# Performance work log

Hardware: AMD Instinct MI355X
Metric: run time of the kernel (lower is better)

## Reference

```python
import jax, jax.numpy as jnp
import numpy as np

SHAPES = ((64, 64), (32, 32), (16, 16), (8, 8))
LEVEL_STARTS = np.concatenate([[0], np.cumsum([h * w for h, w in SHAPES])]).tolist()
N_LEVELS = 4; N_HEADS = 8; N_POINTS = 4; D_MODEL = 256; HEAD_DIM = 32; D_FFN = 1024; NUM_LAYERS = 2
LEN_IN = sum(h * w for h, w in SHAPES)
BATCH = 2


def setup_inputs():
    key = jax.random.key(0)
    ks = iter(jax.random.split(key, 40))
    r = lambda shape, s=1.0: jax.random.normal(next(ks), shape, dtype=jnp.float32) * s
    L = NUM_LAYERS
    return {
        "src": r((BATCH, LEN_IN, D_MODEL)),
        "pos": r((BATCH, LEN_IN, D_MODEL), 0.5),
        "valid_ratios": jnp.ones((BATCH, N_LEVELS, 2), jnp.float32),
        "Wv": r((L, D_MODEL, D_MODEL), 0.05), "bv": jnp.zeros((L, D_MODEL), jnp.float32),
        "Woff": r((L, D_MODEL, N_HEADS * N_LEVELS * N_POINTS * 2), 0.002),
        "boff": r((L, N_HEADS * N_LEVELS * N_POINTS * 2), 0.5),
        "Wa": r((L, D_MODEL, N_HEADS * N_LEVELS * N_POINTS), 0.05),
        "ba": jnp.zeros((L, N_HEADS * N_LEVELS * N_POINTS), jnp.float32),
        "Wo": r((L, D_MODEL, D_MODEL), 0.05), "bo": jnp.zeros((L, D_MODEL), jnp.float32),
        "g1": jnp.ones((L, D_MODEL), jnp.float32), "be1": jnp.zeros((L, D_MODEL), jnp.float32),
        "Wl1": r((L, D_MODEL, D_FFN), 0.05), "bl1": jnp.zeros((L, D_FFN), jnp.float32),
        "Wl2": r((L, D_FFN, D_MODEL), 0.05), "bl2": jnp.zeros((L, D_MODEL), jnp.float32),
        "g2": jnp.ones((L, D_MODEL), jnp.float32), "be2": jnp.zeros((L, D_MODEL), jnp.float32),
    }


def layer_norm(x, g, b, eps=1e-5):
    m = jnp.mean(x, -1, keepdims=True)
    v = jnp.mean(jnp.square(x - m), -1, keepdims=True)
    return (x - m) * jax.lax.rsqrt(v + eps) * g + b


def make_reference_points(valid_ratios):
    # DeformableTransformerEncoder.get_reference_points, vectorized per level
    refs = []
    for lvl, (H, W) in enumerate(SHAPES):
        gy, gx = jnp.meshgrid(jnp.arange(H, dtype=jnp.float32) + 0.5,
                              jnp.arange(W, dtype=jnp.float32) + 0.5, indexing="ij")
        ry = gy.reshape(-1)[None] / (valid_ratios[:, lvl, 1][:, None] * H)
        rx = gx.reshape(-1)[None] / (valid_ratios[:, lvl, 0][:, None] * W)
        refs.append(jnp.stack([rx, ry], -1))  # [N, H*W, 2]
    ref = jnp.concatenate(refs, 1)  # [N, Len, 2]
    return ref[:, :, None, :] * valid_ratios[:, None]  # [N, Len, n_levels, 2]


def ms_deform_attn(query, input_flatten, reference_points, Wv, bv, Woff, boff, Wa, ba, Wo, bo):
    N, Lq, _ = query.shape
    value = (input_flatten @ Wv + bv).reshape(N, -1, N_HEADS, HEAD_DIM)
    off = (query @ Woff + boff).reshape(N, Lq, N_HEADS, N_LEVELS, N_POINTS, 2)
    aw = (query @ Wa + ba).reshape(N, Lq, N_HEADS, N_LEVELS * N_POINTS)
    aw = jax.nn.softmax(aw, -1).reshape(N, Lq, N_HEADS, N_LEVELS, N_POINTS)
    # normalizer is (W, H) per level, as in MSDeformAttn
    normalizer = jnp.array([[w, h] for h, w in SHAPES], jnp.float32)
    loc = reference_points[:, :, None, :, None, :] + off / normalizer[None, None, None, :, None, :]
    acc = jnp.zeros((N, N_HEADS, Lq, HEAD_DIM), query.dtype)
    for lvl, (H, W) in enumerate(SHAPES):
        s = LEVEL_STARTS[lvl]
        val = value[:, s:s + H * W].transpose(0, 2, 1, 3)  # [N, heads, H*W, hd]
        # grid_sample bilinear, align_corners=False, zero padding
        x = loc[:, :, :, lvl, :, 0] * W - 0.5  # [N, Lq, heads, P]
        y = loc[:, :, :, lvl, :, 1] * H - 0.5
        x0 = jnp.floor(x); y0 = jnp.floor(y)
        wx1 = x - x0; wy1 = y - y0
        ix0 = x0.astype(jnp.int32); iy0 = y0.astype(jnp.int32)

        def corner(ix, iy, w):
            valid = (ix >= 0) & (ix < W) & (iy >= 0) & (iy < H)
            idx = jnp.clip(iy, 0, H - 1) * W + jnp.clip(ix, 0, W - 1)
            idx = idx.transpose(0, 2, 1, 3).reshape(N, N_HEADS, Lq * N_POINTS)
            g = jnp.take_along_axis(val, idx[..., None], axis=2).reshape(N, N_HEADS, Lq, N_POINTS, HEAD_DIM)
            w = jnp.where(valid, w, 0.0).transpose(0, 2, 1, 3)  # [N, heads, Lq, P]
            return g * w[..., None]

        sampled = (corner(ix0, iy0, (1 - wx1) * (1 - wy1))
                   + corner(ix0 + 1, iy0, wx1 * (1 - wy1))
                   + corner(ix0, iy0 + 1, (1 - wx1) * wy1)
                   + corner(ix0 + 1, iy0 + 1, wx1 * wy1))
        acc = acc + (sampled * aw[:, :, :, lvl].transpose(0, 2, 1, 3)[..., None]).sum(3)
    out = acc.transpose(0, 2, 1, 3).reshape(N, Lq, D_MODEL)
    return out @ Wo + bo


def reference(src, pos, valid_ratios, Wv, bv, Woff, boff, Wa, ba, Wo, bo,
              g1, be1, Wl1, bl1, Wl2, bl2, g2, be2):
    ref_pts = make_reference_points(valid_ratios)
    out = src
    for l in range(NUM_LAYERS):
        q = out + pos  # with_pos_embed
        attn = ms_deform_attn(q, out, ref_pts, Wv[l], bv[l], Woff[l], boff[l],
                              Wa[l], ba[l], Wo[l], bo[l])
        out = layer_norm(out + attn, g1[l], be1[l])
        ffn = jax.nn.relu(out @ Wl1[l] + bl1[l]) @ Wl2[l] + bl2[l]
        out = layer_norm(out + ffn, g2[l], be2[l])
    return out
```

## Files before the change

### kernel.cpp

```cpp
#include <hip/hip_runtime.h>
#include <math.h>

#define LEN   5440
#define NB    2
#define MROWS (NB * LEN)
#define DM    256
#define NH    8
#define HD    32
#define NLV   4
#define NPT   4
#define DFFN  1024

typedef __attribute__((ext_vector_type(8))) short bf16x8;
typedef __attribute__((ext_vector_type(4))) short bf16x4;
typedef __attribute__((ext_vector_type(4))) float f32x4;

__device__ __forceinline__ short f2bf(float f) {
    union { float f; unsigned u; } cv; cv.f = f;
    unsigned r = cv.u + 0x7fffu + ((cv.u >> 16) & 1u);
    return (short)(r >> 16);
}
__device__ __forceinline__ float bf2f(short s) {
    union { unsigned u; float f; } cv;
    cv.u = ((unsigned)(unsigned short)s) << 16;
    return cv.f;
}

__global__ __launch_bounds__(256) void transpose_convert_all(
    const float* __restrict__ Wv,  const float* __restrict__ Woff,
    const float* __restrict__ Wa,  const float* __restrict__ Wo,
    const float* __restrict__ Wl1, const float* __restrict__ Wl2,
    short* __restrict__ out)
{
    int bx = blockIdx.x;
    int l  = bx / 736;
    int t  = bx % 736;
    const float* src; int K, N; long doff;
    if      (t < 64)  { src = Wv;   K = 256;  N = 256;  doff = 0;      }
    else if (t < 128) { src = Woff; K = 256;  N = 256;  doff = 65536;  t -= 64;  }
    else if (t < 160) { src = Wa;   K = 256;  N = 128;  doff = 131072; t -= 128; }
    else if (t < 224) { src = Wo;   K = 256;  N = 256;  doff = 163840; t -= 160; }
    else if (t < 480) { src = Wl1;  K = 256;  N = 1024; doff = 229376; t -= 224; }
    else              { src = Wl2;  K = 1024; N = 256;  doff = 491520; t -= 480; }
    src += (long)l * K * N;
    short* dst = out + (long)l * 753664 + doff;

    const int ntx = N / 32;
    const int n0 = (t % ntx) * 32, k0 = (t / ntx) * 32;

    __shared__ short T[32][33];
    const int tid = threadIdx.x;
    {
        const int n = tid & 31, kq = tid >> 5;
        #pragma unroll
        for (int i = 0; i < 4; ++i) {
            int k = kq * 4 + i;
            T[n][k] = f2bf(src[(long)(k0 + k) * N + n0 + n]);
        }
    }
    __syncthreads();
    {
        const int k = tid & 31, nq = tid >> 5;
        #pragma unroll
        for (int i = 0; i < 4; ++i) {
            int n = nq * 4 + i;
            dst[(long)(n0 + n) * K + k0 + k] = T[n][k];
        }
    }
}

__global__ __launch_bounds__(256) void convert_src(
    const float4* __restrict__ s4, const float4* __restrict__ p4,
    bf16x4* __restrict__ curb, bf16x4* __restrict__ qb)
{
    const int i = blockIdx.x * 256 + threadIdx.x;
    float4 s = s4[i], p = p4[i];
    bf16x4 c, q;
    c[0] = f2bf(s.x); c[1] = f2bf(s.y); c[2] = f2bf(s.z); c[3] = f2bf(s.w);
    q[0] = f2bf(s.x + p.x); q[1] = f2bf(s.y + p.y);
    q[2] = f2bf(s.z + p.z); q[3] = f2bf(s.w + p.w);
    curb[i] = c; qb[i] = q;
}

template <int BN, int RELU, int OMODE>
__device__ __forceinline__ void gemm_core128(
    short* As, short* Bs,
    const short* __restrict__ A, const short* __restrict__ Wt,
    const float* __restrict__ bias, float* __restrict__ Cf,
    short* __restrict__ Cb,
    int ldc, int m0, int wrow0, int ccol0, int K)
{
    constexpr int NF = BN / 32;
    constexpr int NBJ = BN / 64;
    const int t    = threadIdx.x;
    const int wave = t >> 6, lane = t & 63;
    const int wm   = (wave & 1) * 64;
    const int wn   = (wave >> 1) * (BN / 2);
    const int lm   = lane & 15;
    const int chkg = lane >> 4;
    const int srow = t >> 2;
    const int sc   = t & 3;

    f32x4 acc[4][NF] = {};
    bf16x8 ar[2], br[NBJ];

    #pragma unroll
    for (int j = 0; j < 2; ++j)
        ar[j] = *(const bf16x8*)(A + (long)(m0 + srow + 64 * j) * K + sc * 8);
    #pragma unroll
    for (int j = 0; j < NBJ; ++j)
        br[j] = *(const bf16x8*)(Wt + (long)(wrow0 + srow + 64 * j) * K + sc * 8);

    for (int k0 = 0; k0 < K; k0 += 32) {
        __syncthreads();
        #pragma unroll
        for (int j = 0; j < 2; ++j)
            *(bf16x8*)(&As[(srow + 64 * j) * 40 + sc * 8]) = ar[j];
        #pragma unroll
        for (int j = 0; j < NBJ; ++j)
            *(bf16x8*)(&Bs[(srow + 64 * j) * 40 + sc * 8]) = br[j];
        __syncthreads();

        if (k0 + 32 < K) {
            #pragma unroll
            for (int j = 0; j < 2; ++j)
                ar[j] = *(const bf16x8*)(A + (long)(m0 + srow + 64 * j) * K + k0 + 32 + sc * 8);
            #pragma unroll
            for (int j = 0; j < NBJ; ++j)
                br[j] = *(const bf16x8*)(Wt + (long)(wrow0 + srow + 64 * j) * K + k0 + 32 + sc * 8);
        }

        bf16x8 af[4], bfv[NF];
        #pragma unroll
        for (int s = 0; s < 4; ++s)
            af[s] = *(const bf16x8*)(&As[(wm + s * 16 + lm) * 40 + chkg * 8]);
        #pragma unroll
        for (int u = 0; u < NF; ++u)
            bfv[u] = *(const bf16x8*)(&Bs[(wn + u * 16 + lm) * 40 + chkg * 8]);
        #pragma unroll
        for (int s = 0; s < 4; ++s)
            #pragma unroll
            for (int u = 0; u < NF; ++u)
                acc[s][u] = __builtin_amdgcn_mfma_f32_16x16x32_bf16(
                    af[s], bfv[u], acc[s][u], 0, 0, 0);
    }

    const int col = lane & 15;
    const int rq  = (lane >> 4) * 4;
    #pragma unroll
    for (int s = 0; s < 4; ++s) {
        #pragma unroll
        for (int u = 0; u < NF; ++u) {
            const int gn = ccol0 + wn + u * 16 + col;
            const float bb = bias[gn];
            #pragma unroll
            for (int r = 0; r < 4; ++r) {
                const int gm = m0 + wm + s * 16 + rq + r;
                float v = acc[s][u][r] + bb;
                if (RELU) v = fmaxf(v, 0.f);
                if (OMODE == 0) {
                    Cf[(long)gm * ldc + gn] = v;
                } else if (OMODE == 1) {
                    Cb[(long)gm * ldc + gn] = f2bf(v);
                } else {
                    const int n   = gm / LEN;
                    const int pix = gm - n * LEN;
                    const int h   = gn >> 5, d = gn & 31;
                    Cb[((long)(n * NH + h) * LEN + pix) * 32 + d] = f2bf(v);
                }
            }
        }
    }
}

template <int BN, int RELU, int OMODE>
__global__ __launch_bounds__(256) void gemm128(
    const short* __restrict__ A, const short* __restrict__ Wt,
    const float* __restrict__ bias, float* Cf, short* Cb, int ldc, int K)
{
    __shared__ __align__(16) short As[128 * 40];
    __shared__ __align__(16) short Bs[BN * 40];
    gemm_core128<BN, RELU, OMODE>(As, Bs, A, Wt, bias, Cf, Cb, ldc,
                                  blockIdx.y * 128, blockIdx.x * BN,
                                  blockIdx.x * BN, K);
}

__global__ __launch_bounds__(256) void gemm_qkv128(
    const short* __restrict__ curb, const short* __restrict__ qb,
    const short* __restrict__ Wt, const float* __restrict__ bv,
    const float* __restrict__ boff, const float* __restrict__ ba,
    short* __restrict__ Vb, float* __restrict__ OFF, float* __restrict__ AW)
{
    __shared__ __align__(16) short As[128 * 40];
    __shared__ __align__(16) short Bs[128 * 40];
    const int n0 = blockIdx.x * 128;
    if (n0 < 256) {
        gemm_core128<128, 0, 2>(As, Bs, curb, Wt, bv, (float*)nullptr, Vb,
                                256, blockIdx.y * 128, n0, n0, 256);
    } else if (n0 < 512) {
        gemm_core128<128, 0, 0>(As, Bs, qb, Wt, boff, OFF, (short*)nullptr,
                                256, blockIdx.y * 128, n0, n0 - 256, 256);
    } else {
        gemm_core128<128, 0, 0>(As, Bs, qb, Wt, ba, AW, (short*)nullptr,
                                128, blockIdx.y * 128, n0, n0 - 512, 256);
    }
}

__global__ __launch_bounds__(256) void deform_attn_v3(
    const short* __restrict__ Vb,
    const float* __restrict__ OFF,
    const float* __restrict__ AW,
    const float* __restrict__ vr,
    bf16x4* __restrict__ ATTb)
{
    const int starts[5] = {0, 4096, 5120, 5376, 5440};
    const int dims[4]   = {64, 32, 16, 8};

    const int wave = threadIdx.x >> 6;
    const int lane = threadIdx.x & 63;
    const int h    = lane >> 3;
    const int d4   = lane & 7;

    const int gq = blockIdx.x * 4 + wave;
    const int n  = gq / LEN;
    const int q  = gq % LEN;

    int lq = 3;
    if (q < 4096) lq = 0; else if (q < 5120) lq = 1; else if (q < 5376) lq = 2;
    const int r  = q - starts[lq];
    const int Wq = dims[lq];
    const int gy = r / Wq, gx = r % Wq;
    const float vrxq = vr[(n * NLV + lq) * 2 + 0];
    const float vryq = vr[(n * NLV + lq) * 2 + 1];
    const float rx = (gx + 0.5f) / (vrxq * Wq);
    const float ry = (gy + 0.5f) / (vryq * Wq);

    const long row = (long)n * LEN + q;

    const float* awp = AW + row * 128 + h * 16;
    float a[16];
    float mx = -1e30f;
    #pragma unroll
    for (int i = 0; i < 16; ++i) { a[i] = awp[i]; mx = fmaxf(mx, a[i]); }
    float s = 0.f;
    #pragma unroll
    for (int i = 0; i < 16; ++i) { a[i] = __expf(a[i] - mx); s += a[i]; }
    const float inv = 1.f / s;

    const float* offp = OFF + row * 256 + h * 32;

    float4 acc = {0.f, 0.f, 0.f, 0.f};
    #pragma unroll
    for (int lvl = 0; lvl < NLV; ++lvl) {
        const int Hl = dims[lvl];
        const int Wl = Hl;
        const float fW = (float)Wl;
        const int sb = starts[lvl];
        const float lx = rx * vr[(n * NLV + lvl) * 2 + 0];
        const float ly = ry * vr[(n * NLV + lvl) * 2 + 1];
        const short* vb = Vb + ((long)(n * NH + h) * LEN + sb) * 32 + d4 * 4;
        #pragma unroll
        for (int p = 0; p < NPT; ++p) {
            const float ox = offp[lvl * 8 + p * 2 + 0];
            const float oy = offp[lvl * 8 + p * 2 + 1];
            const float x = fmaf(lx, fW, ox) - 0.5f;
            const float y = fmaf(ly, fW, oy) - 0.5f;
            const float x0f = floorf(x), y0f = floorf(y);
            const int ix0 = (int)x0f, iy0 = (int)y0f;
            const float wx1 = x - x0f, wy1 = y - y0f;
            const float wx0 = 1.f - wx1, wy0 = 1.f - wy1;

            const bool vx0 = (ix0 >= 0)     && (ix0 < Wl);
            const bool vx1 = (ix0 + 1 >= 0) && (ix0 + 1 < Wl);
            const bool vy0 = (iy0 >= 0)     && (iy0 < Hl);
            const bool vy1 = (iy0 + 1 >= 0) && (iy0 + 1 < Hl);
            const int cx0 = min(max(ix0, 0), Wl - 1);
            const int cx1 = min(max(ix0 + 1, 0), Wl - 1);
            const int cy0 = min(max(iy0, 0), Hl - 1);
            const int cy1 = min(max(iy0 + 1, 0), Hl - 1);

            const float w00 = (vx0 && vy0) ? wx0 * wy0 : 0.f;
            const float w10 = (vx1 && vy0) ? wx1 * wy0 : 0.f;
            const float w01 = (vx0 && vy1) ? wx0 * wy1 : 0.f;
            const float w11 = (vx1 && vy1) ? wx1 * wy1 : 0.f;

            const bf16x4 g00 = *(const bf16x4*)(vb + (long)(cy0 * Wl + cx0) * 32);
            const bf16x4 g10 = *(const bf16x4*)(vb + (long)(cy0 * Wl + cx1) * 32);
            const bf16x4 g01 = *(const bf16x4*)(vb + (long)(cy1 * Wl + cx0) * 32);
            const bf16x4 g11 = *(const bf16x4*)(vb + (long)(cy1 * Wl + cx1) * 32);

            const float awv = a[lvl * 4 + p] * inv;
            #pragma unroll
            for (int e = 0; e < 4; ++e) {
                float sv = w00 * bf2f(g00[e]) + w10 * bf2f(g10[e])
                         + w01 * bf2f(g01[e]) + w11 * bf2f(g11[e]);
                (&acc.x)[e] += awv * sv;
            }
        }
    }
    bf16x4 ob;
    ob[0] = f2bf(acc.x); ob[1] = f2bf(acc.y);
    ob[2] = f2bf(acc.z); ob[3] = f2bf(acc.w);
    ATTb[row * 64 + h * 8 + d4] = ob;
}

__global__ __launch_bounds__(256) void add_ln_kernel(
    const float* __restrict__ X, const float* __restrict__ Y,
    const float* __restrict__ g, const float* __restrict__ b,
    float* __restrict__ outf, short* __restrict__ outb,
    short* __restrict__ outq, const float* __restrict__ pos)
{
    const long row = blockIdx.x;
    const int  t   = threadIdx.x;
    const int lane = t & 63, wid = t >> 6;
    __shared__ float red[4];

    float v = X[row * DM + t] + Y[row * DM + t];

    float s = v;
    #pragma unroll
    for (int o = 32; o > 0; o >>= 1) s += __shfl_down(s, o, 64);
    if (lane == 0) red[wid] = s;
    __syncthreads();
    const float mean = (red[0] + red[1] + red[2] + red[3]) * (1.f / DM);
    __syncthreads();

    const float dv = v - mean;
    float s2 = dv * dv;
    #pragma unroll
    for (int o = 32; o > 0; o >>= 1) s2 += __shfl_down(s2, o, 64);
    if (lane == 0) red[wid] = s2;
    __syncthreads();
    const float var = (red[0] + red[1] + red[2] + red[3]) * (1.f / DM);

    const float r = dv * rsqrtf(var + 1e-5f) * g[t] + b[t];
    if (outf) outf[row * DM + t] = r;
    if (outb) outb[row * DM + t] = f2bf(r);
    if (outq) outq[row * DM + t] = f2bf(r + pos[row * DM + t]);
}

extern "C" void kernel_launch(void* const* d_in, const int* in_sizes, int n_in,
                              void* d_out, int out_size, void* d_ws, size_t ws_size,
                              hipStream_t stream)
{
    const float* src = (const float*)d_in[0];
    const float* pos = (const float*)d_in[1];
    const float* vr  = (const float*)d_in[2];
    const float* Wv_   = (const float*)d_in[3];
    const float* bv_   = (const float*)d_in[4];
    const float* Woff_ = (const float*)d_in[5];
    const float* boff_ = (const float*)d_in[6];
    const float* Wa_   = (const float*)d_in[7];
    const float* ba_   = (const float*)d_in[8];
    const float* Wo_   = (const float*)d_in[9];
    const float* bo_   = (const float*)d_in[10];
    const float* g1_   = (const float*)d_in[11];
    const float* be1_  = (const float*)d_in[12];
    const float* Wl1_  = (const float*)d_in[13];
    const float* bl1_  = (const float*)d_in[14];
    const float* Wl2_  = (const float*)d_in[15];
    const float* bl2_  = (const float*)d_in[16];
    const float* g2_   = (const float*)d_in[17];
    const float* be2_  = (const float*)d_in[18];

    const long SZ = (long)MROWS * DM;
    float* ws = (float*)d_ws;
    float* OFF  = ws;
    float* AW   = OFF + SZ;
    float* AO   = AW  + (long)MROWS * 128;
    float* XA   = AO  + SZ;
    float* XB   = XA  + SZ;
    short* Vb   = (short*)(XB + SZ);
    short* curb = Vb   + SZ;
    short* qb   = curb + SZ;
    short* ATTb = qb   + SZ;
    short* XAb  = ATTb + SZ;
    short* FFNb = XAb  + SZ;
    short* Wt   = FFNb + (long)MROWS * DFFN;

    const dim3 blk(256);
    const int GYM = MROWS / 128;

    hipLaunchKernelGGL(transpose_convert_all, dim3(1472), blk, 0, stream,
                       Wv_, Woff_, Wa_, Wo_, Wl1_, Wl2_, Wt);
    hipLaunchKernelGGL(convert_src, dim3(SZ / 4 / 256), blk, 0, stream,
                       (const float4*)src, (const float4*)pos,
                       (bf16x4*)curb, (bf16x4*)qb);

    const float* cur = src;
    for (int l = 0; l < 2; ++l) {
        const short* Wbase = Wt + (long)l * 753664;
        const float* bv   = bv_   + (long)l * DM;
        const float* boff = boff_ + (long)l * 256;
        const float* ba   = ba_   + (long)l * 128;
        const float* bo   = bo_   + (long)l * DM;
        const float* g1   = g1_   + (long)l * DM;
        const float* be1  = be1_  + (long)l * DM;
        const float* bl1  = bl1_  + (long)l * DFFN;
        const float* bl2  = bl2_  + (long)l * DM;
        const float* g2   = g2_   + (long)l * DM;
        const float* be2  = be2_  + (long)l * DM;

        hipLaunchKernelGGL(gemm_qkv128, dim3(5, GYM), blk, 0, stream,
                           curb, qb, Wbase, bv, boff, ba, Vb, OFF, AW);
        hipLaunchKernelGGL(deform_attn_v3, dim3(MROWS / 4), blk, 0, stream,
                           Vb, OFF, AW, vr, (bf16x4*)ATTb);
        hipLaunchKernelGGL((gemm128<64, 0, 0>), dim3(4, GYM), blk, 0, stream,
                           ATTb, Wbase + 163840, bo, AO, (short*)nullptr, 256, 256);
        hipLaunchKernelGGL(add_ln_kernel, dim3(MROWS), blk, 0, stream,
                           cur, AO, g1, be1, XA, XAb, (short*)nullptr,
                           (const float*)nullptr);
        hipLaunchKernelGGL((gemm128<128, 1, 1>), dim3(8, GYM), blk, 0, stream,
                           XAb, Wbase + 229376, bl1, (float*)nullptr, FFNb, 1024, 256);
        hipLaunchKernelGGL((gemm128<64, 0, 0>), dim3(4, GYM), blk, 0, stream,
                           FFNb, Wbase + 491520, bl2, AO, (short*)nullptr, 256, 1024);
        if (l == 0) {
            hipLaunchKernelGGL(add_ln_kernel, dim3(MROWS), blk, 0, stream,
                               XA, AO, g2, be2, XB, curb, qb, pos);
            cur = XB;
        } else {
            hipLaunchKernelGGL(add_ln_kernel, dim3(MROWS), blk, 0, stream,
                               XA, AO, g2, be2, (float*)d_out, (short*)nullptr,
                               (short*)nullptr, (const float*)nullptr);
        }
    }
}
```

Baseline: 325.4 us.

## Fuse output and FFN2 GEMMs with residual add and LayerNorm

Adds a gemm_ln kernel where each block computes a full 32x256 row tile of the N=256 GEMM, then adds bias and the residual and applies LayerNorm in registers using a cross-wave shared-memory reduction. It replaces the separate gemm128 and add_ln_kernel pairs for the attention output projection and the second FFN layer, removing the fp32 AO round-trip and two launches per layer. In exchange the GEMM uses a smaller 32-row M tile with an unpipelined-through-LDS loop, which may lower MFMA efficiency. Variance is now computed as E[x^2]-mean^2 in one pass, which is less numerically robust than the old two-pass form.

After: 315.4 us. 3.1% less time.

```diff
diff --git a/kernel.cpp b/kernel.cpp
--- a/kernel.cpp
+++ b/kernel.cpp
@@ -206,6 +206,120 @@
     }
 }
 
+__global__ __launch_bounds__(256) void gemm_ln(
+    const short* __restrict__ A, const short* __restrict__ Wt,
+    const float* __restrict__ bias, const float* __restrict__ resid,
+    const float* __restrict__ g, const float* __restrict__ be,
+    float* __restrict__ outf, short* __restrict__ outb,
+    short* __restrict__ outq, const float* __restrict__ pos, int K)
+{
+    __shared__ __align__(16) short As[32 * 40];
+    __shared__ __align__(16) short Bs[256 * 40];
+    __shared__ float red[2][32][2];
+
+    const int t    = threadIdx.x;
+    const int wave = t >> 6, lane = t & 63;
+    const int wm   = (wave & 1) * 16;
+    const int wn   = (wave >> 1) * 128;
+    const int lm   = lane & 15;
+    const int chkg = lane >> 4;
+    const int srow = t >> 2;
+    const int sc   = t & 3;
+    const int m0   = blockIdx.x * 32;
+    const bool doA = (t < 128);
+
+    f32x4 acc[8] = {};
+    bf16x8 ar, br[4];
+
+    if (doA) ar = *(const bf16x8*)(A + (long)(m0 + srow) * K + sc * 8);
+    #pragma unroll
+    for (int j = 0; j < 4; ++j)
+        br[j] = *(const bf16x8*)(Wt + (long)(srow + 64 * j) * K + sc * 8);
+
+    for (int k0 = 0; k0 < K; k0 += 32) {
+        __syncthreads();
+        if (doA) *(bf16x8*)(&As[srow * 40 + sc * 8]) = ar;
+        #pragma unroll
+        for (int j = 0; j < 4; ++j)
+            *(bf16x8*)(&Bs[(srow + 64 * j) * 40 + sc * 8]) = br[j];
+        __syncthreads();
+
+        if (k0 + 32 < K) {
+            if (doA) ar = *(const bf16x8*)(A + (long)(m0 + srow) * K + k0 + 32 + sc * 8);
+            #pragma unroll
+            for (int j = 0; j < 4; ++j)
+                br[j] = *(const bf16x8*)(Wt + (long)(srow + 64 * j) * K + k0 + 32 + sc * 8);
+        }
+
+        bf16x8 af = *(const bf16x8*)(&As[(wm + lm) * 40 + chkg * 8]);
+        #pragma unroll
+        for (int u = 0; u < 8; ++u) {
+            bf16x8 bfv = *(const bf16x8*)(&Bs[(wn + u * 16 + lm) * 40 + chkg * 8]);
+            acc[u] = __builtin_amdgcn_mfma_f32_16x16x32_bf16(af, bfv, acc[u], 0, 0, 0);
+        }
+    }
+
+    const int rq = (lane >> 4) * 4;
+    #pragma unroll
+    for (int u = 0; u < 8; ++u) {
+        const int gn = wn + u * 16 + lm;
+        const float bb = bias[gn];
+        #pragma unroll
+        for (int r = 0; r < 4; ++r) {
+            const int gm = m0 + wm + rq + r;
+            acc[u][r] += bb + resid[(long)gm * DM + gn];
+        }
+    }
+
+    float rs[4], r2[4];
+    #pragma unroll
+    for (int r = 0; r < 4; ++r) {
+        float s = 0.f, s2 = 0.f;
+        #pragma unroll
+        for (int u = 0; u < 8; ++u) { const float v = acc[u][r]; s += v; s2 += v * v; }
+        rs[r] = s; r2[r] = s2;
+    }
+    #pragma unroll
+    for (int o = 1; o < 16; o <<= 1) {
+        #pragma unroll
+        for (int r = 0; r < 4; ++r) {
+            rs[r] += __shfl_xor(rs[r], o, 64);
+            r2[r] += __shfl_xor(r2[r], o, 64);
+        }
+    }
+    if (lm == 0) {
+        #pragma unroll
+        for (int r = 0; r < 4; ++r) {
+            red[wave >> 1][wm + rq + r][0] = rs[r];
+            red[wave >> 1][wm + rq + r][1] = r2[r];
+        }
+    }
+    __syncthreads();
+    #pragma unroll
+    for (int r = 0; r < 4; ++r) {
+        const int row = wm + rq + r;
+        const float ts = red[0][row][0] + red[1][row][0];
+        const float t2 = red[0][row][1] + red[1][row][1];
+        const float mean = ts * (1.f / DM);
+        const float var  = t2 * (1.f / DM) - mean * mean;
+        rs[r] = mean;
+        r2[r] = rsqrtf(var + 1e-5f);
+    }
+    #pragma unroll
+    for (int u = 0; u < 8; ++u) {
+        const int gn = wn + u * 16 + lm;
+        const float gg = g[gn], bbe = be[gn];
+        #pragma unroll
+        for (int r = 0; r < 4; ++r) {
+            const int gm = m0 + wm + rq + r;
+            const float o = (acc[u][r] - rs[r]) * r2[r] * gg + bbe;
+            outf[(long)gm * DM + gn] = o;
+            if (outb) outb[(long)gm * DM + gn] = f2bf(o);
+            if (outq) outq[(long)gm * DM + gn] = f2bf(o + pos[(long)gm * DM + gn]);
+        }
+    }
+}
+
 __global__ __launch_bounds__(256) void deform_attn_v3(
     const short* __restrict__ Vb,
     const float* __restrict__ OFF,
@@ -302,41 +416,6 @@
     ob[0] = f2bf(acc.x); ob[1] = f2bf(acc.y);
     ob[2] = f2bf(acc.z); ob[3] = f2bf(acc.w);
     ATTb[row * 64 + h * 8 + d4] = ob;
-}
-
-__global__ __launch_bounds__(256) void add_ln_kernel(
-    const float* __restrict__ X, const float* __restrict__ Y,
-    const float* __restrict__ g, const float* __restrict__ b,
-    float* __restrict__ outf, short* __restrict__ outb,
-    short* __restrict__ outq, const float* __restrict__ pos)
-{
-    const long row = blockIdx.x;
-    const int  t   = threadIdx.x;
-    const int lane = t & 63, wid = t >> 6;
-    __shared__ float red[4];
-
-    float v = X[row * DM + t] + Y[row * DM + t];
-
-    float s = v;
-    #pragma unroll
-    for (int o = 32; o > 0; o >>= 1) s += __shfl_down(s, o, 64);
-    if (lane == 0) red[wid] = s;
-    __syncthreads();
-    const float mean = (red[0] + red[1] + red[2] + red[3]) * (1.f / DM);
-    __syncthreads();
-
-    const float dv = v - mean;
-    float s2 = dv * dv;
-    #pragma unroll
-    for (int o = 32; o > 0; o >>= 1) s2 += __shfl_down(s2, o, 64);
-    if (lane == 0) red[wid] = s2;
-    __syncthreads();
-    const float var = (red[0] + red[1] + red[2] + red[3]) * (1.f / DM);
-
-    const float r = dv * rsqrtf(var + 1e-5f) * g[t] + b[t];
-    if (outf) outf[row * DM + t] = r;
-    if (outb) outb[row * DM + t] = f2bf(r);
-    if (outq) outq[row * DM + t] = f2bf(r + pos[row * DM + t]);
 }
 
 extern "C" void kernel_launch(void* const* d_in, const int* in_sizes, int n_in,
@@ -367,8 +446,7 @@
     float* ws = (float*)d_ws;
     float* OFF  = ws;
     float* AW   = OFF + SZ;
-    float* AO   = AW  + (long)MROWS * 128;
-    float* XA   = AO  + SZ;
+    float* XA   = AW  + (long)MROWS * 128;
     float* XB   = XA  + SZ;
     short* Vb   = (short*)(XB + SZ);
     short* curb = Vb   + SZ;
@@ -380,6 +458,7 @@
 
     const dim3 blk(256);
     const int GYM = MROWS / 128;
+    const int GLN = MROWS / 32;
 
     hipLaunchKernelGGL(transpose_convert_all, dim3(1472), blk, 0, stream,
                        Wv_, Woff_, Wa_, Wo_, Wl1_, Wl2_, Wt);
@@ -405,23 +484,21 @@
                            curb, qb, Wbase, bv, boff, ba, Vb, OFF, AW);
         hipLaunchKernelGGL(deform_attn_v3, dim3(MROWS / 4), blk, 0, stream,
                            Vb, OFF, AW, vr, (bf16x4*)ATTb);
-        hipLaunchKernelGGL((gemm128<64, 0, 0>), dim3(4, GYM), blk, 0, stream,
-                           ATTb, Wbase + 163840, bo, AO, (short*)nullptr, 256, 256);
-        hipLaunchKernelGGL(add_ln_kernel, dim3(MROWS), blk, 0, stream,
-                           cur, AO, g1, be1, XA, XAb, (short*)nullptr,
-                           (const float*)nullptr);
+        hipLaunchKernelGGL(gemm_ln, dim3(GLN), blk, 0, stream,
+                           ATTb, Wbase + 163840, bo, cur, g1, be1,
+                           XA, XAb, (short*)nullptr, (const float*)nullptr, 256);
         hipLaunchKernelGGL((gemm128<128, 1, 1>), dim3(8, GYM), blk, 0, stream,
                            XAb, Wbase + 229376, bl1, (float*)nullptr, FFNb, 1024, 256);
-        hipLaunchKernelGGL((gemm128<64, 0, 0>), dim3(4, GYM), blk, 0, stream,
-                           FFNb, Wbase + 491520, bl2, AO, (short*)nullptr, 256, 1024);
         if (l == 0) {
-            hipLaunchKernelGGL(add_ln_kernel, dim3(MROWS), blk, 0, stream,
-                               XA, AO, g2, be2, XB, curb, qb, pos);
+            hipLaunchKernelGGL(gemm_ln, dim3(GLN), blk, 0, stream,
+                               FFNb, Wbase + 491520, bl2, XA, g2, be2,
+                               XB, curb, qb, pos, 1024);
             cur = XB;
         } else {
-            hipLaunchKernelGGL(add_ln_kernel, dim3(MROWS), blk, 0, stream,
-                               XA, AO, g2, be2, (float*)d_out, (short*)nullptr,
-                               (short*)nullptr, (const float*)nullptr);
-        }
-    }
-}
+            hipLaunchKernelGGL(gemm_ln, dim3(GLN), blk, 0, stream,
+                               FFNb, Wbase + 491520, bl2, XA, g2, be2,
+                               (float*)d_out, (short*)nullptr, (short*)nullptr,
+                               (const float*)nullptr, 1024);
+        }
+    }
+}
```
